# Performance work log

Measured on AMD Instinct MI355X. Metric: run time of the kernel, lower is better.

## Reference

```python
import jax, jax.numpy as jnp
import numpy as np

VOCAB, D_MODEL, DICT, TOP_K = 50257, 512, 16384, 32
N_CONCEPTS, N_RELATIONS = 16, 6
B, S = 1024, 32


def sparse_topk(coeffs, top_k):
    # abs-topk along last dim, keep signed values, scatter to dense
    _, idx = jax.lax.top_k(jnp.abs(coeffs), top_k)          # [B, k]
    signed = jnp.take_along_axis(coeffs, idx, axis=-1)      # [B, k]
    rows = jnp.arange(coeffs.shape[0])[:, None]
    return jnp.zeros_like(coeffs).at[rows, idx].set(signed)


def setup_inputs() -> dict:
    key = jax.random.key(0)
    ks = jax.random.split(key, 16)
    f = lambda k, shape, scale: jax.random.normal(k, shape, dtype=jnp.float32) * scale
    inp = {
        'clean_tokens': jax.random.randint(ks[0], (B, S), 0, VOCAB),
        'noisy_tokens': jax.random.randint(ks[1], (B, S), 0, VOCAB),
        'embedding': f(ks[2], (VOCAB, D_MODEL), 1.0),
        'enc_w1': f(ks[3], (D_MODEL, D_MODEL), D_MODEL ** -0.5),
        'enc_b1': jnp.zeros((D_MODEL,), jnp.float32),
        'enc_w2': f(ks[4], (D_MODEL, D_MODEL), D_MODEL ** -0.5),
        'enc_b2': jnp.zeros((D_MODEL,), jnp.float32),
        'shared_atoms': f(ks[5], (DICT, D_MODEL), 0.04),
        'router_w': f(ks[6], (DICT, D_MODEL), D_MODEL ** -0.5),
        'concept_delta_w': f(ks[7], (DICT, D_MODEL), D_MODEL ** -0.5),
        'relation_delta_w': f(ks[8], (DICT, D_MODEL), D_MODEL ** -0.5),
        'concept_head_w': f(ks[9], (N_CONCEPTS, D_MODEL), D_MODEL ** -0.5),
        'concept_head_b': jnp.zeros((N_CONCEPTS,), jnp.float32),
        'relation_head_w': f(ks[10], (N_RELATIONS, D_MODEL), D_MODEL ** -0.5),
        'relation_head_b': jnp.zeros((N_RELATIONS,), jnp.float32),
    }
    return inp


def reference(clean_tokens, noisy_tokens, embedding, enc_w1, enc_b1, enc_w2, enc_b2,
              shared_atoms, router_w, concept_delta_w, relation_delta_w,
              concept_head_w, concept_head_b, relation_head_w, relation_head_b):
    def pooled(tokens):
        x = embedding[tokens].mean(axis=1)                       # [B, D]
        h = jax.nn.silu(x @ enc_w1.T + enc_b1)
        return h @ enc_w2.T + enc_b2

    def encode(p, delta_w):
        coeffs = p @ router_w.T + 0.3 * (p @ delta_w.T)          # [B, DICT]
        sparse = sparse_topk(coeffs, TOP_K)
        rep = sparse @ shared_atoms                              # [B, D]
        return rep, sparse

    clean_p = pooled(clean_tokens)
    noisy_p = pooled(noisy_tokens)
    c_rep, c_sp = encode(clean_p, concept_delta_w)
    r_rep, r_sp = encode(clean_p, relation_delta_w)
    nc_rep, nc_sp = encode(noisy_p, concept_delta_w)
    nr_rep, nr_sp = encode(noisy_p, relation_delta_w)

    fused_clean = 0.2 * clean_p + 0.9 * c_rep + 0.9 * r_rep
    fused_noisy = 0.2 * noisy_p + 0.9 * nc_rep + 0.9 * nr_rep

    return (fused_clean @ concept_head_w.T + concept_head_b,
            fused_clean @ relation_head_w.T + relation_head_b,
            fused_noisy @ concept_head_w.T + concept_head_b,
            fused_noisy @ relation_head_w.T + relation_head_b,
            c_sp, r_sp, nc_sp, nr_sp)
```

## Files before the change

kernel.cpp:

```cpp
#include <hip/hip_runtime.h>


typedef _Float16 f16x8 __attribute__((ext_vector_type(8)));
typedef _Float16 f16x4 __attribute__((ext_vector_type(4)));
typedef float f32x4 __attribute__((ext_vector_type(4)));

#define OUT_SPARSE 45056
#define SPARSE_PER 16777216

#define ASYNC16(gp, lp) __builtin_amdgcn_global_load_lds(                      \
    (const __attribute__((address_space(1))) void*)(gp),                       \
    (__attribute__((address_space(3))) void*)(lp), 16, 0, 0)

__device__ inline float h2f(unsigned s) {
    _Float16 h = __builtin_bit_cast(_Float16, (unsigned short)(s & 0xFFFFu));
    return (float)h;
}

__global__ __launch_bounds__(128) void pool_kernel(
    const int* __restrict__ ct, const int* __restrict__ nt,
    const float* __restrict__ emb, double* __restrict__ xout)
{
    const int row = blockIdx.x, s = blockIdx.y;
    const int tid = threadIdx.x;
    __shared__ int tk[32];
    const int* t = (s ? nt : ct) + row * 32;
    if (tid < 32) tk[tid] = t[tid];
    __syncthreads();
    const int d = tid * 4;
    double a0 = 0, a1 = 0, a2 = 0, a3 = 0;
    for (int i = 0; i < 32; ++i) {
        const float4 v = *(const float4*)(emb + (size_t)tk[i] * 512 + d);
        a0 += (double)v.x; a1 += (double)v.y; a2 += (double)v.z; a3 += (double)v.w;
    }
    double* o = xout + ((size_t)s * 1024 + row) * 512 + d;
    o[0] = a0 * 0.03125; o[1] = a1 * 0.03125; o[2] = a2 * 0.03125; o[3] = a3 * 0.03125;
}

__global__ __launch_bounds__(256) void enc_gemm(
    const double* __restrict__ A, const float* __restrict__ W,
    const float* __restrict__ bias, double* __restrict__ C,
    _Float16* __restrict__ C16, int act)
{
    __shared__ double Ask[16][68];
    __shared__ double Wsk[16][68];
    const int tid = threadIdx.x;
    const int m0 = blockIdx.y * 64, n0 = blockIdx.x * 64;
    const int ty = tid >> 4, tx = tid & 15;
    const int r = tid >> 2, c4 = (tid & 3) * 4;
    double acc[4][4] = {};
    for (int k0 = 0; k0 < 512; k0 += 16) {
        const double4 av = *(const double4*)(A + (size_t)(m0 + r) * 512 + k0 + c4);
        const float4  wv = *(const float4*) (W + (size_t)(n0 + r) * 512 + k0 + c4);
        __syncthreads();
        Ask[c4 + 0][r] = av.x; Ask[c4 + 1][r] = av.y; Ask[c4 + 2][r] = av.z; Ask[c4 + 3][r] = av.w;
        Wsk[c4 + 0][r] = (double)wv.x; Wsk[c4 + 1][r] = (double)wv.y;
        Wsk[c4 + 2][r] = (double)wv.z; Wsk[c4 + 3][r] = (double)wv.w;
        __syncthreads();
#pragma unroll
        for (int k = 0; k < 16; ++k) {
            const double4 a = *(const double4*)&Ask[k][ty * 4];
            const double4 b = *(const double4*)&Wsk[k][tx * 4];
            const double aa[4] = {a.x, a.y, a.z, a.w};
            const double bb[4] = {b.x, b.y, b.z, b.w};
#pragma unroll
            for (int i = 0; i < 4; ++i)
#pragma unroll
                for (int j = 0; j < 4; ++j) acc[i][j] += aa[i] * bb[j];
        }
    }
#pragma unroll
    for (int i = 0; i < 4; ++i) {
        const int row = m0 + ty * 4 + i;
#pragma unroll
        for (int j = 0; j < 4; ++j) {
            const int col = n0 + tx * 4 + j;
            double v = acc[i][j] + (double)bias[col];
            if (act) v = v / (1.0 + exp(-v));
            C[(size_t)row * 512 + col] = v;
            if (C16) C16[(size_t)row * 512 + col] = (_Float16)v;
        }
    }
}

__global__ __launch_bounds__(256) void combine_kernel(
    const float* __restrict__ router, const float* __restrict__ cd,
    const float* __restrict__ rd, _Float16* __restrict__ wc,
    _Float16* __restrict__ wr)
{
    const size_t i = ((size_t)blockIdx.x * 256 + threadIdx.x) * 4;
    if (i >= (size_t)16384 * 512) return;
    const float4 r = *(const float4*)(router + i);
    const float4 c = *(const float4*)(cd + i);
    const float4 d = *(const float4*)(rd + i);
    f16x4 hc = { (_Float16)(r.x + 0.3f * c.x), (_Float16)(r.y + 0.3f * c.y),
                 (_Float16)(r.z + 0.3f * c.z), (_Float16)(r.w + 0.3f * c.w) };
    f16x4 hr = { (_Float16)(r.x + 0.3f * d.x), (_Float16)(r.y + 0.3f * d.y),
                 (_Float16)(r.z + 0.3f * d.z), (_Float16)(r.w + 0.3f * d.w) };
    *(f16x4*)(wc + i) = hc;
    *(f16x4*)(wr + i) = hr;
}

__global__ __launch_bounds__(256) void approx_gemm(
    const _Float16* __restrict__ P, const _Float16* __restrict__ Wc,
    const _Float16* __restrict__ Wr, float* __restrict__ outf)
{
    __shared__ _Float16 As[128 * 32];
    __shared__ _Float16 Bs[128 * 32];
    __shared__ _Float16 Cst[128 * 128];

    const int tid = threadIdx.x;
    const int q = blockIdx.z;
    const int n0 = blockIdx.x * 128, m0 = blockIdx.y * 128;
    const _Float16* A = P + (size_t)(q >> 1) * 524288;
    const _Float16* B = (q & 1) ? Wr : Wc;

    const int lane = tid & 63, w = tid >> 6;
    const int wm = w & 1, wn = w >> 1;
    const int lr = lane & 15, lk = lane >> 4;

    const int ch0 = w * 2, ch1 = w * 2 + 1;
    const int lrow = lane >> 2, lh = (lane & 3) * 8;
    const _Float16* Ag0 = A + (size_t)(m0 + ch0 * 16 + lrow) * 512 + lh;
    const _Float16* Ag1 = A + (size_t)(m0 + ch1 * 16 + lrow) * 512 + lh;
    const _Float16* Bg0 = B + (size_t)(n0 + ch0 * 16 + lrow) * 512 + lh;
    const _Float16* Bg1 = B + (size_t)(n0 + ch1 * 16 + lrow) * 512 + lh;
    _Float16* Al0 = As + ch0 * 512;
    _Float16* Al1 = As + ch1 * 512;
    _Float16* Bl0 = Bs + ch0 * 512;
    _Float16* Bl1 = Bs + ch1 * 512;

    const f32x4 zero = {0.f, 0.f, 0.f, 0.f};
    f32x4 acc[4][4];
#pragma unroll
    for (int i = 0; i < 4; ++i)
#pragma unroll
        for (int j = 0; j < 4; ++j) acc[i][j] = zero;

    for (int kt = 0; kt < 16; ++kt) {
        const int k0 = kt * 32;
        __syncthreads();
        ASYNC16(Ag0 + k0, Al0);
        ASYNC16(Ag1 + k0, Al1);
        ASYNC16(Bg0 + k0, Bl0);
        ASYNC16(Bg1 + k0, Bl1);
        __syncthreads();
        f16x8 af[4], bf[4];
#pragma unroll
        for (int i = 0; i < 4; ++i) af[i] = *(const f16x8*)(As + (wm * 64 + i * 16 + lr) * 32 + lk * 8);
#pragma unroll
        for (int j = 0; j < 4; ++j) bf[j] = *(const f16x8*)(Bs + (wn * 64 + j * 16 + lr) * 32 + lk * 8);
#pragma unroll
        for (int i = 0; i < 4; ++i)
#pragma unroll
            for (int j = 0; j < 4; ++j)
                acc[i][j] = __builtin_amdgcn_mfma_f32_16x16x32_f16(af[i], bf[j], acc[i][j], 0, 0, 0);
    }
    __syncthreads();
#pragma unroll
    for (int i = 0; i < 4; ++i)
#pragma unroll
        for (int j = 0; j < 4; ++j)
#pragma unroll
            for (int rr = 0; rr < 4; ++rr)
                Cst[(wm * 64 + i * 16 + lk * 4 + rr) * 128 + (wn * 64 + j * 16 + lr)] =
                    (_Float16)acc[i][j][rr];
    __syncthreads();
    unsigned short* ob = (unsigned short*)outf + (size_t)2 * OUT_SPARSE + (size_t)q * 2 * SPARSE_PER;
#pragma unroll
    for (int p = 0; p < 8; ++p) {
        const int cc = p * 256 + tid;
        const int rl = cc >> 4;
        const int chh = (cc & 15) * 8;
        const float4 v = *(const float4*)(Cst + rl * 128 + chh);
        *(float4*)(ob + (size_t)(m0 + rl) * 32768 + n0 + chh) = v;
    }
}

__global__ __launch_bounds__(256) void select_kernel(
    const double* __restrict__ pw, const float* __restrict__ router,
    const float* __restrict__ cdelta, const float* __restrict__ rdelta,
    const float* __restrict__ atoms, float* __restrict__ outf,
    float* __restrict__ repw)
{
    constexpr int NCAP = 160, NRE = 64;
    const int row = blockIdx.x, q = blockIdx.y;
    const int pset = q >> 1;
    const int tid = threadIdx.x;

    __shared__ unsigned hist[1024];
    __shared__ unsigned pscan[256];
    __shared__ double prow[512];
    __shared__ int cidx[NCAP];
    __shared__ unsigned short ckey[NCAP];
    __shared__ int r64i[NRE];
    __shared__ double cval[NRE];
    __shared__ float selv[32];
    __shared__ int seli[32];
    __shared__ float wred[4];
    __shared__ int cnt, bstar;
    __shared__ unsigned cutk_s;

    float* orow = outf + (size_t)OUT_SPARSE + (size_t)q * SPARSE_PER + (size_t)row * 16384;
    const double* prg = pw + ((size_t)pset * 1024 + row) * 512;

    for (int b = tid; b < 1024; b += 256) hist[b] = 0;
    if (tid == 0) { cnt = 0; bstar = -1; }
    prow[tid] = prg[tid];
    prow[tid + 256] = prg[tid + 256];

    uint4 rv[8];
    const uint4* ar4 = (const uint4*)orow;
#pragma unroll
    for (int p = 0; p < 8; ++p) rv[p] = ar4[p * 256 + tid];

    float ss = 0.f;
#pragma unroll
    for (int p = 0; p < 8; ++p) {
        const unsigned uu[4] = {rv[p].x, rv[p].y, rv[p].z, rv[p].w};
#pragma unroll
        for (int e = 0; e < 4; ++e) {
            const float f0 = h2f(uu[e]), f1 = h2f(uu[e] >> 16);
            ss = fmaf(f0, f0, ss);
            ss = fmaf(f1, f1, ss);
        }
    }
    for (int sh = 32; sh > 0; sh >>= 1) ss += __shfl_down(ss, sh);
    const int w = tid >> 6, lane = tid & 63;
    if (lane == 0) wred[w] = ss;
    __syncthreads();
    if (tid == 0) {
        const float sig = sqrtf((wred[0] + wred[1] + wred[2] + wred[3]) * (1.f / 16384.f));
        const _Float16 h = (_Float16)(2.0f * sig);
        cutk_s = (unsigned)__builtin_bit_cast(unsigned short, h) & 0x7FFFu;
    }
    __syncthreads();
    const unsigned cutk = cutk_s;

#pragma unroll
    for (int p = 0; p < 8; ++p) {
        const unsigned uu[4] = {rv[p].x, rv[p].y, rv[p].z, rv[p].w};
#pragma unroll
        for (int e = 0; e < 4; ++e) {
            const unsigned k0 = uu[e] & 0x7FFFu, k1 = (uu[e] >> 16) & 0x7FFFu;
            if (k0 >= cutk) atomicAdd(&hist[k0 >> 5], 1u);
            if (k1 >= cutk) atomicAdd(&hist[k1 >> 5], 1u);
        }
    }
    __syncthreads();

    const float4 z4 = {0.f, 0.f, 0.f, 0.f};
    float4* o4 = (float4*)orow;
#pragma unroll
    for (int p = 0; p < 16; ++p) o4[p * 256 + tid] = z4;

    const unsigned h0 = hist[tid * 4], h1 = hist[tid * 4 + 1];
    const unsigned h2 = hist[tid * 4 + 2], h3 = hist[tid * 4 + 3];
    const unsigned l3 = h3, l2 = h2 + l3, l1 = h1 + l2, l0 = h0 + l1;
    pscan[tid] = l0;
    __syncthreads();
    for (int s = 1; s < 256; s <<= 1) {
        const unsigned v = (tid + s < 256) ? pscan[tid + s] : 0u;
        __syncthreads();
        pscan[tid] += v;
        __syncthreads();
    }
    {
        const unsigned above = (tid < 255) ? pscan[tid + 1] : 0u;
        int best = -1;
        if (l0 + above >= 64u) best = tid * 4;
        if (l1 + above >= 64u) best = tid * 4 + 1;
        if (l2 + above >= 64u) best = tid * 4 + 2;
        if (l3 + above >= 64u) best = tid * 4 + 3;
        if (best >= 0) atomicMax(&bstar, best);
    }
    __syncthreads();
    const unsigned kmin = (unsigned)(bstar < 0 ? 0 : bstar) << 5;

#pragma unroll
    for (int p = 0; p < 8; ++p) {
        const unsigned uu[4] = {rv[p].x, rv[p].y, rv[p].z, rv[p].w};
        const int base = (p * 256 + tid) * 8;
#pragma unroll
        for (int e = 0; e < 4; ++e) {
            const unsigned k0 = uu[e] & 0x7FFFu, k1 = (uu[e] >> 16) & 0x7FFFu;
            if (k0 >= kmin) { const int pos = atomicAdd(&cnt, 1); if (pos < NCAP) { cidx[pos] = base + e * 2;     ckey[pos] = (unsigned short)k0; } }
            if (k1 >= kmin) { const int pos = atomicAdd(&cnt, 1); if (pos < NCAP) { cidx[pos] = base + e * 2 + 1; ckey[pos] = (unsigned short)k1; } }
        }
    }
    __syncthreads();
    const int nc = min(cnt, NCAP);

    for (int p = tid; p < nc; p += 256) {
        const unsigned mk = ckey[p];
        const int mi = cidx[p];
        int rr = 0;
        for (int j = 0; j < nc; ++j) {
            const unsigned kj = ckey[j];
            rr += (kj > mk || (kj == mk && cidx[j] < mi)) ? 1 : 0;
        }
        if (rr < NRE) r64i[rr] = mi;
    }
    __syncthreads();

    const float* drow = (q & 1) ? rdelta : cdelta;
    for (int c = w; c < NRE; c += 4) {
        const int idx = r64i[c];
        const float4* rp4 = (const float4*)(router + (size_t)idx * 512);
        const float4* dp4 = (const float4*)(drow + (size_t)idx * 512);
        const float4 r0 = rp4[lane * 2], r1 = rp4[lane * 2 + 1];
        const float4 d0 = dp4[lane * 2], d1 = dp4[lane * 2 + 1];
        const double* pv = prow + lane * 8;
        double aR = pv[0] * (double)r0.x + pv[1] * (double)r0.y + pv[2] * (double)r0.z + pv[3] * (double)r0.w
                  + pv[4] * (double)r1.x + pv[5] * (double)r1.y + pv[6] * (double)r1.z + pv[7] * (double)r1.w;
        double aD = pv[0] * (double)d0.x + pv[1] * (double)d0.y + pv[2] * (double)d0.z + pv[3] * (double)d0.w
                  + pv[4] * (double)d1.x + pv[5] * (double)d1.y + pv[6] * (double)d1.z + pv[7] * (double)d1.w;
        for (int sh = 32; sh > 0; sh >>= 1) { aR += __shfl_down(aR, sh); aD += __shfl_down(aD, sh); }
        if (lane == 0) cval[c] = aR + 0.3 * aD;
    }
    __syncthreads();

    if (tid < NRE) {
        const double av = fabs(cval[tid]);
        const int mi = r64i[tid];
        int rr = 0;
        for (int j = 0; j < NRE; ++j) {
            const double aj = fabs(cval[j]);
            rr += (aj > av || (aj == av && r64i[j] < mi)) ? 1 : 0;
        }
        if (rr < 32) {
            const float fv = (float)cval[tid];
            selv[rr] = fv; seli[rr] = mi;
            orow[mi] = fv;
        }
    }
    __syncthreads();

    double a0 = 0, a1 = 0;
    for (int k = 0; k < 32; ++k) {
        const double v = (double)selv[k];
        const float* ar = atoms + (size_t)seli[k] * 512;
        a0 += v * (double)ar[tid];
        a1 += v * (double)ar[tid + 256];
    }
    float* rp = repw + ((size_t)q * 1024 + row) * 512;
    rp[tid] = (float)a0;
    rp[tid + 256] = (float)a1;
}

__global__ __launch_bounds__(256) void heads_kernel(
    const double* __restrict__ pw, const float* __restrict__ repw,
    const float* __restrict__ chw, const float* __restrict__ chb,
    const float* __restrict__ rhw, const float* __restrict__ rhb,
    float* __restrict__ out)
{
    const int row = blockIdx.x, s = blockIdx.y;
    const int tid = threadIdx.x;
    __shared__ double fused[512];
    const double* pr = pw + ((size_t)s * 1024 + row) * 512;
    const float* rc = repw + ((size_t)(s * 2 + 0) * 1024 + row) * 512;
    const float* rr = repw + ((size_t)(s * 2 + 1) * 1024 + row) * 512;
    for (int d = tid; d < 512; d += 256)
        fused[d] = 0.2 * pr[d] + 0.9 * (double)rc[d] + 0.9 * (double)rr[d];
    __syncthreads();
    const int w = tid >> 6, lane = tid & 63;
    for (int o = w; o < 22; o += 4) {
        const float* hw = (o < 16) ? (chw + (size_t)o * 512) : (rhw + (size_t)(o - 16) * 512);
        double acc = 0;
#pragma unroll
        for (int j = 0; j < 8; ++j) acc += fused[lane + 64 * j] * (double)hw[lane + 64 * j];
        for (int sh = 32; sh > 0; sh >>= 1) acc += __shfl_down(acc, sh);
        if (lane == 0) {
            if (o < 16) out[(s ? 22528 : 0) + row * 16 + o] = (float)(acc + (double)chb[o]);
            else        out[(s ? 38912 : 16384) + row * 6 + (o - 16)] = (float)(acc + (double)rhb[o - 16]);
        }
    }
}

extern "C" void kernel_launch(void* const* d_in, const int* in_sizes, int n_in,
                              void* d_out, int out_size, void* d_ws, size_t ws_size,
                              hipStream_t stream)
{
    const int*   ctok   = (const int*)d_in[0];
    const int*   ntok   = (const int*)d_in[1];
    const float* emb    = (const float*)d_in[2];
    const float* w1     = (const float*)d_in[3];
    const float* b1     = (const float*)d_in[4];
    const float* w2     = (const float*)d_in[5];
    const float* b2     = (const float*)d_in[6];
    const float* atoms  = (const float*)d_in[7];
    const float* router = (const float*)d_in[8];
    const float* cdelta = (const float*)d_in[9];
    const float* rdelta = (const float*)d_in[10];
    const float* chw    = (const float*)d_in[11];
    const float* chb    = (const float*)d_in[12];
    const float* rhw    = (const float*)d_in[13];
    const float* rhb    = (const float*)d_in[14];
    float* out = (float*)d_out;

    double*    xw   = (double*)d_ws;
    double*    hw   = xw + 1048576;
    double*    pw   = hw + 1048576;
    float*     repw = (float*)(pw + 1048576);
    _Float16*  pf16 = (_Float16*)(repw + 2097152);
    _Float16*  wcw  = pf16 + 1048576;
    _Float16*  wrw  = wcw + 8388608;

    pool_kernel<<<dim3(1024, 2), 128, 0, stream>>>(ctok, ntok, emb, xw);
    enc_gemm<<<dim3(8, 32), 256, 0, stream>>>(xw, w1, b1, hw, (_Float16*)nullptr, 1);
    enc_gemm<<<dim3(8, 32), 256, 0, stream>>>(hw, w2, b2, pw, pf16, 0);
    combine_kernel<<<8192, 256, 0, stream>>>(router, cdelta, rdelta, wcw, wrw);
    approx_gemm<<<dim3(128, 8, 4), 256, 0, stream>>>(pf16, wcw, wrw, out);
    select_kernel<<<dim3(1024, 4), 256, 0, stream>>>(pw, router, cdelta, rdelta, atoms, out, repw);
    heads_kernel<<<dim3(1024, 2), 256, 0, stream>>>(pw, repw, chw, chb, rhw, rhb, out);
}
```

Measured before the change: 873.4 us.

## Emit per-tile top candidates from approx GEMM instead of full fp16 score matrix

The approximate GEMM now does per-row, per-tile candidate filtering in its epilogue (local RMS threshold, up to 32 packed key/index entries per 128-column tile). It writes only these compact candidates instead of the full fp16 coefficient matrix. The select kernel builds its histogram from the candidates, and the combined fp32 weights are precomputed so refinement does one dot product instead of two. The sparse outputs are zeroed once by a separate kernel and scattered in the heads kernel. This cuts large intermediate traffic, but the per-tile cap of 32 could drop true top-k entries, and the output buffer is used as scratch before being zeroed.

Result: no change. 876.7 us (+0.4%).

```diff
diff --git a/kernel.cpp b/kernel.cpp
--- a/kernel.cpp
+++ b/kernel.cpp
@@ -86,28 +86,33 @@
 __global__ __launch_bounds__(256) void combine_kernel(
     const float* __restrict__ router, const float* __restrict__ cd,
     const float* __restrict__ rd, _Float16* __restrict__ wc,
-    _Float16* __restrict__ wr)
+    _Float16* __restrict__ wr, float* __restrict__ wcf,
+    float* __restrict__ wrf)
 {
     const size_t i = ((size_t)blockIdx.x * 256 + threadIdx.x) * 4;
     if (i >= (size_t)16384 * 512) return;
     const float4 r = *(const float4*)(router + i);
     const float4 c = *(const float4*)(cd + i);
     const float4 d = *(const float4*)(rd + i);
-    f16x4 hc = { (_Float16)(r.x + 0.3f * c.x), (_Float16)(r.y + 0.3f * c.y),
-                 (_Float16)(r.z + 0.3f * c.z), (_Float16)(r.w + 0.3f * c.w) };
-    f16x4 hr = { (_Float16)(r.x + 0.3f * d.x), (_Float16)(r.y + 0.3f * d.y),
-                 (_Float16)(r.z + 0.3f * d.z), (_Float16)(r.w + 0.3f * d.w) };
+    const float4 fc = { r.x + 0.3f * c.x, r.y + 0.3f * c.y, r.z + 0.3f * c.z, r.w + 0.3f * c.w };
+    const float4 fr = { r.x + 0.3f * d.x, r.y + 0.3f * d.y, r.z + 0.3f * d.z, r.w + 0.3f * d.w };
+    f16x4 hc = { (_Float16)fc.x, (_Float16)fc.y, (_Float16)fc.z, (_Float16)fc.w };
+    f16x4 hr = { (_Float16)fr.x, (_Float16)fr.y, (_Float16)fr.z, (_Float16)fr.w };
     *(f16x4*)(wc + i) = hc;
     *(f16x4*)(wr + i) = hr;
+    *(float4*)(wcf + i) = fc;
+    *(float4*)(wrf + i) = fr;
 }
 
 __global__ __launch_bounds__(256) void approx_gemm(
     const _Float16* __restrict__ P, const _Float16* __restrict__ Wc,
-    const _Float16* __restrict__ Wr, float* __restrict__ outf)
-{
-    __shared__ _Float16 As[128 * 32];
-    __shared__ _Float16 Bs[128 * 32];
+    const _Float16* __restrict__ Wr, unsigned* __restrict__ candg)
+{
+    __shared__ _Float16 ABs[8192];
     __shared__ _Float16 Cst[128 * 128];
+    __shared__ unsigned ecnt[128];
+    _Float16* As = ABs;
+    _Float16* Bs = ABs + 4096;
 
     const int tid = threadIdx.x;
     const int q = blockIdx.z;
@@ -165,23 +170,56 @@
             for (int rr = 0; rr < 4; ++rr)
                 Cst[(wm * 64 + i * 16 + lk * 4 + rr) * 128 + (wn * 64 + j * 16 + lr)] =
                     (_Float16)acc[i][j][rr];
-    __syncthreads();
-    unsigned short* ob = (unsigned short*)outf + (size_t)2 * OUT_SPARSE + (size_t)q * 2 * SPARSE_PER;
-#pragma unroll
-    for (int p = 0; p < 8; ++p) {
-        const int cc = p * 256 + tid;
-        const int rl = cc >> 4;
-        const int chh = (cc & 15) * 8;
-        const float4 v = *(const float4*)(Cst + rl * 128 + chh);
-        *(float4*)(ob + (size_t)(m0 + rl) * 32768 + n0 + chh) = v;
+    if (tid < 128) ecnt[tid] = 0;
+    __syncthreads();
+
+    const int r = tid >> 1, h = tid & 1;
+    const unsigned* cr = (const unsigned*)(Cst + r * 128 + h * 64);
+    float ss = 0.f;
+#pragma unroll
+    for (int j = 0; j < 32; ++j) {
+        const unsigned u = cr[j];
+        const float f0 = h2f(u), f1 = h2f(u >> 16);
+        ss = fmaf(f0, f0, fmaf(f1, f1, ss));
+    }
+    ss += __shfl_xor(ss, 1);
+    const _Float16 hc = (_Float16)(2.0f * sqrtf(ss * (1.f / 128.f)));
+    const unsigned cutk = (unsigned)__builtin_bit_cast(unsigned short, hc) & 0x7FFFu;
+    unsigned* emit = (unsigned*)ABs;
+    const int colbase = n0 + h * 64;
+#pragma unroll
+    for (int j = 0; j < 32; ++j) {
+        const unsigned u = cr[j];
+        const unsigned k0 = u & 0x7FFFu, k1 = (u >> 16) & 0x7FFFu;
+        if (k0 >= cutk && k0) {
+            const unsigned pos = atomicAdd(&ecnt[r], 1u);
+            if (pos < 32u) emit[r * 32 + pos] = (k0 << 16) | (unsigned)(16383 - (colbase + 2 * j));
+        }
+        if (k1 >= cutk && k1) {
+            const unsigned pos = atomicAdd(&ecnt[r], 1u);
+            if (pos < 32u) emit[r * 32 + pos] = (k1 << 16) | (unsigned)(16383 - (colbase + 2 * j + 1));
+        }
+    }
+    __syncthreads();
+    {
+        const unsigned c = min(ecnt[r], 32u);
+#pragma unroll
+        for (int s2 = 0; s2 < 16; ++s2) {
+            const unsigned sl = (unsigned)(h * 16 + s2);
+            if (sl >= c) emit[r * 32 + sl] = 0u;
+        }
+        unsigned* eg = candg + (((size_t)q * 1024 + m0 + r) * 128 + blockIdx.x) * 32;
+        const uint4* e4 = (const uint4*)(emit + r * 32 + h * 16);
+        uint4* g4 = (uint4*)(eg + h * 16);
+        g4[0] = e4[0]; g4[1] = e4[1]; g4[2] = e4[2]; g4[3] = e4[3];
     }
 }
 
 __global__ __launch_bounds__(256) void select_kernel(
-    const double* __restrict__ pw, const float* __restrict__ router,
-    const float* __restrict__ cdelta, const float* __restrict__ rdelta,
-    const float* __restrict__ atoms, float* __restrict__ outf,
-    float* __restrict__ repw)
+    const double* __restrict__ pw, const float* __restrict__ wcf,
+    const float* __restrict__ wrf, const unsigned* __restrict__ candg,
+    const float* __restrict__ atoms, float* __restrict__ selvw,
+    int* __restrict__ seliw, float* __restrict__ repw)
 {
     constexpr int NCAP = 160, NRE = 64;
     const int row = blockIdx.x, q = blockIdx.y;
@@ -191,68 +229,35 @@
     __shared__ unsigned hist[1024];
     __shared__ unsigned pscan[256];
     __shared__ double prow[512];
-    __shared__ int cidx[NCAP];
-    __shared__ unsigned short ckey[NCAP];
+    __shared__ unsigned cent[NCAP];
     __shared__ int r64i[NRE];
     __shared__ double cval[NRE];
     __shared__ float selv[32];
     __shared__ int seli[32];
-    __shared__ float wred[4];
     __shared__ int cnt, bstar;
-    __shared__ unsigned cutk_s;
-
-    float* orow = outf + (size_t)OUT_SPARSE + (size_t)q * SPARSE_PER + (size_t)row * 16384;
+
     const double* prg = pw + ((size_t)pset * 1024 + row) * 512;
+    const unsigned* crow = candg + ((size_t)q * 1024 + row) * 4096;
 
     for (int b = tid; b < 1024; b += 256) hist[b] = 0;
     if (tid == 0) { cnt = 0; bstar = -1; }
+    if (tid < NRE) r64i[tid] = 0;
     prow[tid] = prg[tid];
     prow[tid + 256] = prg[tid + 256];
 
-    uint4 rv[8];
-    const uint4* ar4 = (const uint4*)orow;
-#pragma unroll
-    for (int p = 0; p < 8; ++p) rv[p] = ar4[p * 256 + tid];
-
-    float ss = 0.f;
-#pragma unroll
-    for (int p = 0; p < 8; ++p) {
-        const unsigned uu[4] = {rv[p].x, rv[p].y, rv[p].z, rv[p].w};
-#pragma unroll
-        for (int e = 0; e < 4; ++e) {
-            const float f0 = h2f(uu[e]), f1 = h2f(uu[e] >> 16);
-            ss = fmaf(f0, f0, ss);
-            ss = fmaf(f1, f1, ss);
-        }
-    }
-    for (int sh = 32; sh > 0; sh >>= 1) ss += __shfl_down(ss, sh);
-    const int w = tid >> 6, lane = tid & 63;
-    if (lane == 0) wred[w] = ss;
-    __syncthreads();
-    if (tid == 0) {
-        const float sig = sqrtf((wred[0] + wred[1] + wred[2] + wred[3]) * (1.f / 16384.f));
-        const _Float16 h = (_Float16)(2.0f * sig);
-        cutk_s = (unsigned)__builtin_bit_cast(unsigned short, h) & 0x7FFFu;
-    }
-    __syncthreads();
-    const unsigned cutk = cutk_s;
-
-#pragma unroll
-    for (int p = 0; p < 8; ++p) {
-        const unsigned uu[4] = {rv[p].x, rv[p].y, rv[p].z, rv[p].w};
-#pragma unroll
-        for (int e = 0; e < 4; ++e) {
-            const unsigned k0 = uu[e] & 0x7FFFu, k1 = (uu[e] >> 16) & 0x7FFFu;
-            if (k0 >= cutk) atomicAdd(&hist[k0 >> 5], 1u);
-            if (k1 >= cutk) atomicAdd(&hist[k1 >> 5], 1u);
-        }
-    }
-    __syncthreads();
-
-    const float4 z4 = {0.f, 0.f, 0.f, 0.f};
-    float4* o4 = (float4*)orow;
-#pragma unroll
-    for (int p = 0; p < 16; ++p) o4[p * 256 + tid] = z4;
+    uint4 cv[4];
+#pragma unroll
+    for (int p = 0; p < 4; ++p) cv[p] = ((const uint4*)crow)[p * 256 + tid];
+    __syncthreads();
+
+#pragma unroll
+    for (int p = 0; p < 4; ++p) {
+        const unsigned ee[4] = {cv[p].x, cv[p].y, cv[p].z, cv[p].w};
+#pragma unroll
+        for (int e = 0; e < 4; ++e)
+            if (ee[e]) atomicAdd(&hist[ee[e] >> 21], 1u);
+    }
+    __syncthreads();
 
     const unsigned h0 = hist[tid * 4], h1 = hist[tid * 4 + 1];
     const unsigned h2 = hist[tid * 4 + 2], h3 = hist[tid * 4 + 3];
@@ -275,48 +280,41 @@
         if (best >= 0) atomicMax(&bstar, best);
     }
     __syncthreads();
-    const unsigned kmin = (unsigned)(bstar < 0 ? 0 : bstar) << 5;
-
-#pragma unroll
-    for (int p = 0; p < 8; ++p) {
-        const unsigned uu[4] = {rv[p].x, rv[p].y, rv[p].z, rv[p].w};
-        const int base = (p * 256 + tid) * 8;
+    const unsigned kmin = (unsigned)(bstar < 0 ? 1 : bstar) << 5;
+
+#pragma unroll
+    for (int p = 0; p < 4; ++p) {
+        const unsigned ee[4] = {cv[p].x, cv[p].y, cv[p].z, cv[p].w};
 #pragma unroll
         for (int e = 0; e < 4; ++e) {
-            const unsigned k0 = uu[e] & 0x7FFFu, k1 = (uu[e] >> 16) & 0x7FFFu;
-            if (k0 >= kmin) { const int pos = atomicAdd(&cnt, 1); if (pos < NCAP) { cidx[pos] = base + e * 2;     ckey[pos] = (unsigned short)k0; } }
-            if (k1 >= kmin) { const int pos = atomicAdd(&cnt, 1); if (pos < NCAP) { cidx[pos] = base + e * 2 + 1; ckey[pos] = (unsigned short)k1; } }
+            if (ee[e] && (ee[e] >> 16) >= kmin) {
+                const int pos = atomicAdd(&cnt, 1);
+                if (pos < NCAP) cent[pos] = ee[e];
+            }
         }
     }
     __syncthreads();
     const int nc = min(cnt, NCAP);
 
     for (int p = tid; p < nc; p += 256) {
-        const unsigned mk = ckey[p];
-        const int mi = cidx[p];
+        const unsigned e = cent[p];
         int rr = 0;
-        for (int j = 0; j < nc; ++j) {
-            const unsigned kj = ckey[j];
-            rr += (kj > mk || (kj == mk && cidx[j] < mi)) ? 1 : 0;
-        }
-        if (rr < NRE) r64i[rr] = mi;
-    }
-    __syncthreads();
-
-    const float* drow = (q & 1) ? rdelta : cdelta;
+        for (int j = 0; j < nc; ++j) rr += (cent[j] > e) ? 1 : 0;
+        if (rr < NRE) r64i[rr] = 16383 - (int)(e & 0xFFFFu);
+    }
+    __syncthreads();
+
+    const float* wsel = (q & 1) ? wrf : wcf;
+    const int w = tid >> 6, lane = tid & 63;
     for (int c = w; c < NRE; c += 4) {
         const int idx = r64i[c];
-        const float4* rp4 = (const float4*)(router + (size_t)idx * 512);
-        const float4* dp4 = (const float4*)(drow + (size_t)idx * 512);
+        const float4* rp4 = (const float4*)(wsel + (size_t)idx * 512);
         const float4 r0 = rp4[lane * 2], r1 = rp4[lane * 2 + 1];
-        const float4 d0 = dp4[lane * 2], d1 = dp4[lane * 2 + 1];
         const double* pv = prow + lane * 8;
         double aR = pv[0] * (double)r0.x + pv[1] * (double)r0.y + pv[2] * (double)r0.z + pv[3] * (double)r0.w
                   + pv[4] * (double)r1.x + pv[5] * (double)r1.y + pv[6] * (double)r1.z + pv[7] * (double)r1.w;
-        double aD = pv[0] * (double)d0.x + pv[1] * (double)d0.y + pv[2] * (double)d0.z + pv[3] * (double)d0.w
-                  + pv[4] * (double)d1.x + pv[5] * (double)d1.y + pv[6] * (double)d1.z + pv[7] * (double)d1.w;
-        for (int sh = 32; sh > 0; sh >>= 1) { aR += __shfl_down(aR, sh); aD += __shfl_down(aD, sh); }
-        if (lane == 0) cval[c] = aR + 0.3 * aD;
+        for (int sh = 32; sh > 0; sh >>= 1) aR += __shfl_down(aR, sh);
+        if (lane == 0) cval[c] = aR;
     }
     __syncthreads();
 
@@ -328,13 +326,14 @@
             const double aj = fabs(cval[j]);
             rr += (aj > av || (aj == av && r64i[j] < mi)) ? 1 : 0;
         }
-        if (rr < 32) {
-            const float fv = (float)cval[tid];
-            selv[rr] = fv; seli[rr] = mi;
-            orow[mi] = fv;
-        }
-    }
-    __syncthreads();
+        if (rr < 32) { selv[rr] = (float)cval[tid]; seli[rr] = mi; }
+    }
+    __syncthreads();
+    if (tid < 32) {
+        const size_t sb = ((size_t)q * 1024 + row) * 32 + tid;
+        selvw[sb] = selv[tid];
+        seliw[sb] = seli[tid];
+    }
 
     double a0 = 0, a1 = 0;
     for (int k = 0; k < 32; ++k) {
@@ -348,15 +347,31 @@
     rp[tid + 256] = (float)a1;
 }
 
+__global__ __launch_bounds__(256) void zero_kernel(float4* __restrict__ p, unsigned n4)
+{
+    const float4 z = {0.f, 0.f, 0.f, 0.f};
+    unsigned i = blockIdx.x * 256u + threadIdx.x;
+    const unsigned stride = gridDim.x * 256u;
+    for (; i < n4; i += stride) p[i] = z;
+}
+
 __global__ __launch_bounds__(256) void heads_kernel(
     const double* __restrict__ pw, const float* __restrict__ repw,
     const float* __restrict__ chw, const float* __restrict__ chb,
     const float* __restrict__ rhw, const float* __restrict__ rhb,
+    const float* __restrict__ selvw, const int* __restrict__ seliw,
     float* __restrict__ out)
 {
     const int row = blockIdx.x, s = blockIdx.y;
     const int tid = threadIdx.x;
     __shared__ double fused[512];
+
+    if (tid < 64) {
+        const int qq = s * 2 + (tid >> 5), k = tid & 31;
+        const size_t sb = ((size_t)qq * 1024 + row) * 32 + k;
+        out[(size_t)OUT_SPARSE + (size_t)qq * SPARSE_PER + (size_t)row * 16384 + (size_t)seliw[sb]] = selvw[sb];
+    }
+
     const double* pr = pw + ((size_t)s * 1024 + row) * 512;
     const float* rc = repw + ((size_t)(s * 2 + 0) * 1024 + row) * 512;
     const float* rr = repw + ((size_t)(s * 2 + 1) * 1024 + row) * 512;
@@ -365,10 +380,10 @@
     __syncthreads();
     const int w = tid >> 6, lane = tid & 63;
     for (int o = w; o < 22; o += 4) {
-        const float* hw = (o < 16) ? (chw + (size_t)o * 512) : (rhw + (size_t)(o - 16) * 512);
+        const float* hw2 = (o < 16) ? (chw + (size_t)o * 512) : (rhw + (size_t)(o - 16) * 512);
         double acc = 0;
 #pragma unroll
-        for (int j = 0; j < 8; ++j) acc += fused[lane + 64 * j] * (double)hw[lane + 64 * j];
+        for (int j = 0; j < 8; ++j) acc += fused[lane + 64 * j] * (double)hw2[lane + 64 * j];
         for (int sh = 32; sh > 0; sh >>= 1) acc += __shfl_down(acc, sh);
         if (lane == 0) {
             if (o < 16) out[(s ? 22528 : 0) + row * 16 + o] = (float)(acc + (double)chb[o]);
@@ -398,6 +413,10 @@
     const float* rhb    = (const float*)d_in[14];
     float* out = (float*)d_out;
 
+    float*    wcf   = out + OUT_SPARSE;
+    float*    wrf   = wcf + 8388608;
+    unsigned* candg = (unsigned*)(wrf + 8388608);
+
     double*    xw   = (double*)d_ws;
     double*    hw   = xw + 1048576;
     double*    pw   = hw + 1048576;
@@ -405,12 +424,15 @@
     _Float16*  pf16 = (_Float16*)(repw + 2097152);
     _Float16*  wcw  = pf16 + 1048576;
     _Float16*  wrw  = wcw + 8388608;
+    float*     selvw = (float*)hw;
+    int*       seliw = (int*)(selvw + 131072);
 
     pool_kernel<<<dim3(1024, 2), 128, 0, stream>>>(ctok, ntok, emb, xw);
     enc_gemm<<<dim3(8, 32), 256, 0, stream>>>(xw, w1, b1, hw, (_Float16*)nullptr, 1);
     enc_gemm<<<dim3(8, 32), 256, 0, stream>>>(hw, w2, b2, pw, pf16, 0);
-    combine_kernel<<<8192, 256, 0, stream>>>(router, cdelta, rdelta, wcw, wrw);
-    approx_gemm<<<dim3(128, 8, 4), 256, 0, stream>>>(pf16, wcw, wrw, out);
-    select_kernel<<<dim3(1024, 4), 256, 0, stream>>>(pw, router, cdelta, rdelta, atoms, out, repw);
-    heads_kernel<<<dim3(1024, 2), 256, 0, stream>>>(pw, repw, chw, chb, rhw, rhb, out);
-}
+    combine_kernel<<<8192, 256, 0, stream>>>(router, cdelta, rdelta, wcw, wrw, wcf, wrf);
+    approx_gemm<<<dim3(128, 8, 4), 256, 0, stream>>>(pf16, wcw, wrw, candg);
+    select_kernel<<<dim3(1024, 4), 256, 0, stream>>>(pw, wcf, wrf, candg, atoms, selvw, seliw, repw);
+    zero_kernel<<<2048, 256, 0, stream>>>((float4*)(out + OUT_SPARSE), (unsigned)SPARSE_PER);
+    heads_kernel<<<dim3(1024, 2), 256, 0, stream>>>(pw, repw, chw, chb, rhw, rhb, selvw, seliw, out);
+}
```
